# Performance work log

Measured on AMD Instinct MI355X. Metric: run time of the kernel, lower is better.

## Reference

```python
import jax, jax.numpy as jnp
import numpy as np

T, N, E, IN_DIM, OUT_DIM, K = 4, 50000, 800000, 128, 128, 3


def setup_inputs() -> dict:
    key = jax.random.key(0)
    ks = jax.random.split(key, 6)
    x = jax.random.normal(ks[0], (T, N, IN_DIM), dtype=jnp.float32)
    edge_row = jax.random.randint(ks[1], (E,), 0, N, dtype=jnp.int64)
    edge_col = jax.random.randint(ks[2], (E,), 0, N, dtype=jnp.int64)
    edge_val = jax.random.uniform(ks[3], (E,), dtype=jnp.float32)
    # xavier_uniform per [in,out] slice: bound = sqrt(6/(in+out))
    bound = float(np.sqrt(6.0 / (IN_DIM + OUT_DIM)))
    weight = jax.random.uniform(ks[4], (T, K, IN_DIM, OUT_DIM), dtype=jnp.float32,
                                minval=-bound, maxval=bound)
    bias = jnp.zeros((T, OUT_DIM), dtype=jnp.float32)
    return {"x": x, "edge_row": edge_row, "edge_col": edge_col,
            "edge_val": edge_val, "weight": weight, "bias": bias}


def _spmm_batched(edge_row, edge_col, edge_val, h):
    # h: [T, N, C]; sparse A (COO) applied to flattened [N, T*C] features
    t, n, c = h.shape
    h_flat = jnp.transpose(h, (1, 0, 2)).reshape(n, t * c)      # [N, T*C]
    msg = edge_val[:, None] * h_flat[edge_col]                  # [E, T*C]
    out = jax.ops.segment_sum(msg, edge_row, num_segments=n)    # [N, T*C]
    return jnp.transpose(out.reshape(n, t, c), (1, 0, 2))       # [T, N, C]


def reference(x, edge_row, edge_col, edge_val, weight, bias):
    # Chebyshev recurrence: T_0 = x, T_1 = L x, T_k = 2 L T_{k-1} - T_{k-2}
    tx_0 = x
    out = jnp.einsum('tni,tio->tno', tx_0, weight[:, 0])
    tx_1 = _spmm_batched(edge_row, edge_col, edge_val, x)
    out = out + jnp.einsum('tni,tio->tno', tx_1, weight[:, 1])
    for k in range(2, K):
        tx_2 = 2.0 * _spmm_batched(edge_row, edge_col, edge_val, tx_1) - tx_0
        out = out + jnp.einsum('tni,tio->tno', tx_2, weight[:, k])
        tx_0, tx_1 = tx_1, tx_2
    return out + bias[:, None, :]
```

## Files before the change

kernel.cpp:

```cpp
#include <hip/hip_runtime.h>
#include <hip/hip_bf16.h>

#define T_ 4
#define N_ 50000
#define E_ 800000
#define C_ 128
#define K_ 3
#define TC_ 512
#define UNROLL_ 16

typedef __hip_bfloat16 bf16;
typedef __attribute__((ext_vector_type(4))) float f32x4;
typedef __attribute__((ext_vector_type(8))) short bf16x8;
typedef __attribute__((ext_vector_type(4))) short s16x4;

__device__ inline short bf16bits(float f) {
    bf16 h = __float2bfloat16(f);
    union { bf16 h; short s; } u; u.h = h; return u.s;
}
__device__ inline float bf16f(short s) {
    union { bf16 h; short s; } u; u.s = s; return __bfloat162float(u.h);
}


__global__ void count_kernel(const int* __restrict__ row, int* __restrict__ counts) {
    int e = blockIdx.x * blockDim.x + threadIdx.x;
    if (e < E_) atomicAdd(&counts[row[e]], 1);
}

__global__ __launch_bounds__(1024) void scan_kernel(const int* __restrict__ counts,
                                                    int* __restrict__ starts,
                                                    int* __restrict__ cursors) {
    __shared__ int wsum[16];
    __shared__ int carry_s;
    int tid = threadIdx.x;
    int wave = tid >> 6, lane = tid & 63;
    if (tid == 0) carry_s = 0;
    __syncthreads();
    for (int base = 0; base < N_; base += 1024) {
        int i = base + tid;
        int v = (i < N_) ? counts[i] : 0;
        int s = v;
        #pragma unroll
        for (int off = 1; off < 64; off <<= 1) {
            int u = __shfl_up(s, off, 64);
            if (lane >= off) s += u;
        }
        if (lane == 63) wsum[wave] = s;
        __syncthreads();
        if (wave == 0) {
            int w = (lane < 16) ? wsum[lane] : 0;
            #pragma unroll
            for (int off = 1; off < 16; off <<= 1) {
                int u = __shfl_up(w, off, 64);
                if (lane >= off) w += u;
            }
            if (lane < 16) wsum[lane] = w;
        }
        __syncthreads();
        int carry = carry_s;
        int wbase = (wave == 0) ? 0 : wsum[wave - 1];
        int incl = carry + wbase + s;
        if (i < N_) {
            starts[i]  = incl - v;
            cursors[i] = incl - v;
        }
        __syncthreads();
        if (tid == 1023) carry_s = incl;
        __syncthreads();
    }
    if (tid == 0) starts[N_] = carry_s;
}

__global__ void scatter_kernel(const int* __restrict__ row, const int* __restrict__ col,
                               const float* __restrict__ val, int* __restrict__ cursors,
                               int* __restrict__ scol, float* __restrict__ sval) {
    int e = blockIdx.x * blockDim.x + threadIdx.x;
    if (e < E_) {
        int p = atomicAdd(&cursors[row[e]], 1);
        scol[p] = col[e];
        sval[p] = val[e];
    }
}


__global__ __launch_bounds__(256) void convert_kernel(const float* __restrict__ x,
                                                      bf16* __restrict__ xb) {
    int t   = blockIdx.y;
    int idx = blockIdx.x * 256 + threadIdx.x;
    int n = idx >> 5, q = idx & 31;
    f32x4 v = *(const f32x4*)(x + ((size_t)t * N_ + n) * C_ + q * 4);
    s16x4 o;
    #pragma unroll
    for (int j = 0; j < 4; ++j) o[j] = bf16bits(v[j]);
    *(s16x4*)(xb + (size_t)n * TC_ + t * C_ + q * 4) = o;
}


__global__ __launch_bounds__(256) void prep_w_kernel(const float* __restrict__ weight,
                                                     bf16* __restrict__ Wt) {
    __shared__ float lds[32][33];
    int b = blockIdx.x;
    int ts = b >> 4, tile = b & 15;
    int t = ts / 3, kk = ts % 3;
    int it = (tile >> 2) * 32, ot = (tile & 3) * 32;
    int tx = threadIdx.x & 31, ty = threadIdx.x >> 5;
    const float* W  = weight + ((size_t)t * K_ + kk) * C_ * C_;
    const float* W2 = weight + ((size_t)t * K_ + 2) * C_ * C_;
    #pragma unroll
    for (int r = 0; r < 4; ++r) {
        int i = it + ty + r * 8, o = ot + tx;
        float w = W[(size_t)i * C_ + o];
        if (kk == 0)      w -= W2[(size_t)i * C_ + o];
        else if (kk == 2) w *= 2.f;
        lds[ty + r * 8][tx] = w;
    }
    __syncthreads();
    #pragma unroll
    for (int r = 0; r < 4; ++r) {
        int o = ot + ty + r * 8, i = it + tx;
        Wt[((size_t)ts * C_ + o) * C_ + i] = __float2bfloat16(lds[tx][ty + r * 8]);
    }
}


__global__ __launch_bounds__(128) void spmm_kernel(const int* __restrict__ starts,
                                                   const int* __restrict__ scol,
                                                   const float* __restrict__ sval,
                                                   const bf16* __restrict__ src,
                                                   bf16* __restrict__ dst) {
    int n   = blockIdx.x;
    int ch  = threadIdx.x * 4;
    int s  = starts[n];
    int e1 = starts[n + 1];
    const bf16* sb = src + ch;
    f32x4 acc = {0.f, 0.f, 0.f, 0.f};
    for (int e = s; e < e1; e += UNROLL_) {
        int   cc[UNROLL_];
        float vv[UNROLL_];
        #pragma unroll
        for (int j = 0; j < UNROLL_; ++j) {
            int ee = e + j;
            bool ok = ee < e1;
            cc[j] = ok ? scol[ee] : 0;
            vv[j] = ok ? sval[ee] : 0.f;
        }
        s16x4 g[UNROLL_];
        #pragma unroll
        for (int j = 0; j < UNROLL_; ++j)
            g[j] = *(const s16x4*)(sb + (size_t)cc[j] * TC_);
        #pragma unroll
        for (int j = 0; j < UNROLL_; ++j) {
            #pragma unroll
            for (int q = 0; q < 4; ++q)
                acc[q] += vv[j] * bf16f(g[j][q]);
        }
    }
    s16x4 o;
    #pragma unroll
    for (int j = 0; j < 4; ++j) o[j] = bf16bits(acc[j]);
    *(s16x4*)(dst + (size_t)n * TC_ + ch) = o;
}


__global__ __launch_bounds__(256) void gemm_kernel(const float* __restrict__ x,
                                                   const bf16* __restrict__ tx1b,
                                                   const bf16* __restrict__ ub,
                                                   const bf16* __restrict__ Wt,
                                                   const float* __restrict__ bias,
                                                   float* __restrict__ out) {
    int t  = blockIdx.y;
    int m0 = blockIdx.x * 128;
    int tid  = threadIdx.x;
    int wave = tid >> 6, lane = tid & 63;
    int l15 = lane & 15, l4 = lane >> 4;
    int krow = l4 * 8;

    f32x4 acc[2][8];
    #pragma unroll
    for (int i = 0; i < 2; ++i)
        #pragma unroll
        for (int j = 0; j < 8; ++j) acc[i][j] = (f32x4){0.f, 0.f, 0.f, 0.f};

    size_t tslice = (size_t)t * N_ * C_;
    int row[2];
    #pragma unroll
    for (int mf = 0; mf < 2; ++mf) {
        int gr = m0 + wave * 32 + mf * 16 + l15;
        row[mf] = gr < N_ ? gr : N_ - 1;
    }
    const bf16* wt = Wt + (size_t)t * 3 * C_ * C_;

    #pragma unroll
    for (int sid = 0; sid < 3; ++sid) {
        #pragma unroll
        for (int kk = 0; kk < 4; ++kk) {
            int i0 = kk * 32;
            const bf16* wb = wt + (size_t)sid * C_ * C_ + i0 + krow;
            bf16x8 bfr[8];
            #pragma unroll
            for (int nf = 0; nf < 8; ++nf)
                bfr[nf] = *(const bf16x8*)(wb + (size_t)(nf * 16 + l15) * C_);
            bf16x8 a[2];
            if (sid == 0) {
                #pragma unroll
                for (int mf = 0; mf < 2; ++mf) {
                    const float* p = x + tslice + (size_t)row[mf] * C_ + i0 + krow;
                    f32x4 u0 = *(const f32x4*)p;
                    f32x4 u1 = *(const f32x4*)(p + 4);
                    bf16x8 av;
                    #pragma unroll
                    for (int j = 0; j < 4; ++j) { av[j] = bf16bits(u0[j]); av[j + 4] = bf16bits(u1[j]); }
                    a[mf] = av;
                }
            } else {
                const bf16* src = (sid == 1) ? tx1b : ub;
                #pragma unroll
                for (int mf = 0; mf < 2; ++mf)
                    a[mf] = *(const bf16x8*)(src + (size_t)row[mf] * TC_ + t * C_ + i0 + krow);
            }
            #pragma unroll
            for (int mf = 0; mf < 2; ++mf)
                #pragma unroll
                for (int nf = 0; nf < 8; ++nf)
                    acc[mf][nf] = __builtin_amdgcn_mfma_f32_16x16x32_bf16(a[mf], bfr[nf], acc[mf][nf], 0, 0, 0);
        }
    }

    const float* bs = bias + (size_t)t * C_;
    float* ot = out + tslice;
    #pragma unroll
    for (int nf = 0; nf < 8; ++nf) {
        int gc = nf * 16 + l15;
        float bv = bs[gc];
        #pragma unroll
        for (int mf = 0; mf < 2; ++mf) {
            #pragma unroll
            for (int reg = 0; reg < 4; ++reg) {
                int gr = m0 + wave * 32 + mf * 16 + l4 * 4 + reg;
                if (gr < N_) ot[(size_t)gr * C_ + gc] = acc[mf][nf][reg] + bv;
            }
        }
    }
}


extern "C" void kernel_launch(void* const* d_in, const int* in_sizes, int n_in,
                              void* d_out, int out_size, void* d_ws, size_t ws_size,
                              hipStream_t stream) {
    const float* x      = (const float*)d_in[0];
    const int*   erow   = (const int*)d_in[1];
    const int*   ecol   = (const int*)d_in[2];
    const float* eval   = (const float*)d_in[3];
    const float* weight = (const float*)d_in[4];
    const float* bias   = (const float*)d_in[5];
    float* out = (float*)d_out;

    char* ws = (char*)d_ws;
    size_t off = 0;
    auto alloc = [&](size_t bytes) -> void* {
        void* p = ws + off;
        off += (bytes + 255) & ~(size_t)255;
        return p;
    };
    int*   counts  = (int*)alloc((N_ + 1) * sizeof(int));
    int*   starts  = (int*)alloc((N_ + 1) * sizeof(int));
    int*   cursors = (int*)alloc((size_t)N_ * sizeof(int));
    int*   scol    = (int*)alloc((size_t)E_ * sizeof(int));
    float* sval    = (float*)alloc((size_t)E_ * sizeof(float));
    bf16*  bufA    = (bf16*)alloc((size_t)N_ * TC_ * sizeof(bf16));
    bf16*  bufB    = (bf16*)alloc((size_t)N_ * TC_ * sizeof(bf16));
    bf16*  Wt      = (bf16*)alloc((size_t)T_ * K_ * C_ * C_ * sizeof(bf16));

    hipMemsetAsync(counts, 0, (N_ + 1) * sizeof(int), stream);
    count_kernel<<<(E_ + 255) / 256, 256, 0, stream>>>(erow, counts);
    scan_kernel<<<1, 1024, 0, stream>>>(counts, starts, cursors);
    scatter_kernel<<<(E_ + 255) / 256, 256, 0, stream>>>(erow, ecol, eval, cursors, scol, sval);
    prep_w_kernel<<<T_ * K_ * 16, 256, 0, stream>>>(weight, Wt);
    dim3 cg(N_ * 32 / 256, T_);
    convert_kernel<<<cg, 256, 0, stream>>>(x, bufA);
    spmm_kernel<<<N_, 128, 0, stream>>>(starts, scol, sval, bufA, bufB);
    spmm_kernel<<<N_, 128, 0, stream>>>(starts, scol, sval, bufB, bufA);
    dim3 g((N_ + 127) / 128, T_);
    gemm_kernel<<<g, 256, 0, stream>>>(x, bufB, bufA, Wt, bias, out);
}
```

Baseline: 674.1 us.

## Stage GEMM weight slices in LDS and double the block row tile

The GEMM now cooperatively loads each 128x128 bf16 weight slice into shared memory, with register prefetch of the next slice, instead of having every wave read its weight fragments from global memory. The block grows to 512 threads covering 256 rows so each staged slice is reused by more waves. This cuts redundant global/L2 weight traffic but adds barriers and LDS use, and it halves the number of blocks. The GEMM is only part of a pipeline dominated by the SpMM passes.

```diff
diff --git a/kernel.cpp b/kernel.cpp
--- a/kernel.cpp
+++ b/kernel.cpp
@@ -8,6 +8,7 @@
 #define K_ 3
 #define TC_ 512
 #define UNROLL_ 16
+#define GROWS_ 256
 
 typedef __hip_bfloat16 bf16;
 typedef __attribute__((ext_vector_type(4))) float f32x4;
@@ -163,19 +164,23 @@
 }
 
 
-__global__ __launch_bounds__(256) void gemm_kernel(const float* __restrict__ x,
+__global__ __launch_bounds__(512) void gemm_kernel(const float* __restrict__ x,
                                                    const bf16* __restrict__ tx1b,
                                                    const bf16* __restrict__ ub,
                                                    const bf16* __restrict__ Wt,
                                                    const float* __restrict__ bias,
                                                    float* __restrict__ out) {
+    __shared__ __align__(16) short Bs[128][136];
     int t  = blockIdx.y;
-    int m0 = blockIdx.x * 128;
+    int m0 = blockIdx.x * GROWS_;
     int tid  = threadIdx.x;
     int wave = tid >> 6, lane = tid & 63;
     int l15 = lane & 15, l4 = lane >> 4;
     int krow = l4 * 8;
 
+    int sr = tid >> 4;
+    int ss = (tid & 15) * 8;
+
     f32x4 acc[2][8];
     #pragma unroll
     for (int i = 0; i < 2; ++i)
@@ -191,16 +196,30 @@
     }
     const bf16* wt = Wt + (size_t)t * 3 * C_ * C_;
 
+    int4 pf[4];
+    #pragma unroll
+    for (int i = 0; i < 4; ++i)
+        pf[i] = *(const int4*)(wt + (size_t)(i * 32 + sr) * C_ + ss);
+    #pragma unroll
+    for (int i = 0; i < 4; ++i)
+        *(int4*)&Bs[i * 32 + sr][ss] = pf[i];
+    __syncthreads();
+
     #pragma unroll
     for (int sid = 0; sid < 3; ++sid) {
+        if (sid < 2) {
+            const bf16* wn = wt + (size_t)(sid + 1) * C_ * C_;
+            #pragma unroll
+            for (int i = 0; i < 4; ++i)
+                pf[i] = *(const int4*)(wn + (size_t)(i * 32 + sr) * C_ + ss);
+        }
         #pragma unroll
         for (int kk = 0; kk < 4; ++kk) {
             int i0 = kk * 32;
-            const bf16* wb = wt + (size_t)sid * C_ * C_ + i0 + krow;
             bf16x8 bfr[8];
             #pragma unroll
             for (int nf = 0; nf < 8; ++nf)
-                bfr[nf] = *(const bf16x8*)(wb + (size_t)(nf * 16 + l15) * C_);
+                bfr[nf] = *(bf16x8*)&Bs[nf * 16 + l15][i0 + krow];
             bf16x8 a[2];
             if (sid == 0) {
                 #pragma unroll
@@ -225,6 +244,13 @@
                 for (int nf = 0; nf < 8; ++nf)
                     acc[mf][nf] = __builtin_amdgcn_mfma_f32_16x16x32_bf16(a[mf], bfr[nf], acc[mf][nf], 0, 0, 0);
         }
+        __syncthreads();
+        if (sid < 2) {
+            #pragma unroll
+            for (int i = 0; i < 4; ++i)
+                *(int4*)&Bs[i * 32 + sr][ss] = pf[i];
+            __syncthreads();
+        }
     }
 
     const float* bs = bias + (size_t)t * C_;
@@ -281,6 +307,6 @@
     convert_kernel<<<cg, 256, 0, stream>>>(x, bufA);
     spmm_kernel<<<N_, 128, 0, stream>>>(starts, scol, sval, bufA, bufB);
     spmm_kernel<<<N_, 128, 0, stream>>>(starts, scol, sval, bufB, bufA);
-    dim3 g((N_ + 127) / 128, T_);
-    gemm_kernel<<<g, 256, 0, stream>>>(x, bufB, bufA, Wt, bias, out);
-}
+    dim3 g((N_ + GROWS_ - 1) / GROWS_, T_);
+    gemm_kernel<<<g, 512, 0, stream>>>(x, bufB, bufA, Wt, bias, out);
+}
```

Result: faster. 658.0 us (-2.4%).
